# Optimization experiments

Measured on AMD Instinct MI355X. Metric: run time of the kernel, lower is better.

The kernel has to match this reference:

```python
import jax, jax.numpy as jnp
import numpy as np

B = 2; D = 256; NH = 8; NL = 4; HD = D // NH
K = 2; P = K * K; NV = 4; DFF = 1024
SHAPES = ((128, 128), (64, 64), (32, 32), (16, 16))
LV = sum(h * w for h, w in SHAPES)
START = np.cumsum([0] + [h * w for h, w in SHAPES])[:-1].tolist()
EPS = 1e-5

# fixed 2x2 sampling kernel, matching _create_kernel_indices (even kernel branch)
_ind = np.linspace(-0.5, 0.5, K)
_ii, _jj = np.meshgrid(_ind, _ind, indexing='ij')
KERNEL = jnp.asarray(np.stack([_jj, _ii], -1).reshape(-1, 2) / K, jnp.float32)  # (P,2)


def _layer_norm(x, w, b):
    m = x.mean(-1, keepdims=True)
    v = ((x - m) ** 2).mean(-1, keepdims=True)
    return (x - m) * jax.lax.rsqrt(v + EPS) * w + b


def _box_attention(query, value, ref_windows, vpw, vpb, opw, opb, boxw, boxb, attw, attb):
    b, lq, _ = query.shape
    # value projection, split into heads: (b, NH, LV, HD)
    v = (value @ vpw.T + vpb).reshape(b, LV, NH, HD).transpose(0, 2, 1, 3)

    # attention weights: softmax over all (level, point) jointly per head
    aw = query @ attw.T + attb
    aw = jax.nn.softmax(aw.reshape(b, lq, NH, NL * P), -1).reshape(b, lq, NH, NL, P)

    # where to attend (with_rotation=False -> 4 offset variables, angle from ref)
    ob = (query @ boxw.T + boxb).reshape(b, lq, NH, NL, NV)
    rw = ref_windows[:, :, None, None, :]                    # (b,lq,1,1,7)
    ref_boxes = rw[..., jnp.array([0, 1, 3, 4])]
    angles = jnp.broadcast_to(rw[..., 6:7], (b, lq, NH, NL, 1))
    boxes = ref_boxes + ob / 8.0 * ref_boxes[..., jnp.array([2, 3, 2, 3])]
    center = boxes[..., None, :2]                            # (b,lq,NH,NL,1,2)
    size = boxes[..., None, 2:]
    c, s = jnp.cos(angles), jnp.sin(angles)
    rot = jnp.stack([c, -s, s, c], -1).reshape(b, lq, NH, NL, 1, 2, 2)
    g = KERNEL * jax.nn.relu(size)                           # (b,lq,NH,NL,P,2)
    grid = center + (g[..., None, :] * rot).sum(-1)          # (b,lq,NH,NL,P,2)

    # multi-level bilinear sampling (= grid_sample align_corners=False, zero pad)
    bidx = jnp.arange(b)[:, None, None, None]
    hidx = jnp.arange(NH)[None, None, :, None]
    out = jnp.zeros((b, lq, NH, HD), v.dtype)
    for lvl, (H, W) in enumerate(SHAPES):
        st = START[lvl]
        vl = v[:, :, st:st + H * W]                          # (b,NH,HW,HD)
        loc = grid[:, :, :, lvl]                             # (b,lq,NH,P,2)
        x = loc[..., 0] * W - 0.5
        y = loc[..., 1] * H - 0.5
        x0f = jnp.floor(x); y0f = jnp.floor(y)
        wx = x - x0f; wy = y - y0f
        x0 = x0f.astype(jnp.int32); y0 = y0f.astype(jnp.int32)
        acc = jnp.zeros((b, lq, NH, P, HD), v.dtype)
        corners = ((0, 0, (1 - wx) * (1 - wy)), (1, 0, wx * (1 - wy)),
                   (0, 1, (1 - wx) * wy), (1, 1, wx * wy))
        for dx, dy, wgt in corners:
            xi = x0 + dx; yi = y0 + dy
            valid = (xi >= 0) & (xi < W) & (yi >= 0) & (yi < H)
            idx = jnp.clip(yi, 0, H - 1) * W + jnp.clip(xi, 0, W - 1)
            samp = vl[bidx, hidx, idx]                       # (b,lq,NH,P,HD)
            acc = acc + (wgt * valid)[..., None] * samp
        out = out + jnp.einsum('blhp,blhpd->blhd', aw[:, :, :, lvl], acc)
    return out.reshape(b, lq, D) @ opw.T + opb


def setup_inputs() -> dict:
    key = jax.random.key(0)
    ks = jax.random.split(key, 20)
    def nrm(k, shape, fan_in):
        return jax.random.normal(k, shape, jnp.float32) * (1.0 / np.sqrt(fan_in))
    rw = jax.random.uniform(ks[2], (B, LV, 7), jnp.float32)
    # keep window sizes (cols 3,4,5) modest, like real BEV reference windows
    rw = rw.at[..., 3:6].multiply(0.2)
    return {
        'src': jax.random.normal(ks[0], (B, LV, D), jnp.float32),
        'pos': jax.random.normal(ks[1], (B, LV, D), jnp.float32),
        'src_shape': jnp.asarray(SHAPES, jnp.int32),
        'src_start_idx': jnp.asarray(START, jnp.int32),
        'ref_windows': rw,
        'vpw': nrm(ks[3], (D, D), D), 'vpb': jnp.zeros((D,), jnp.float32),
        'opw': nrm(ks[4], (D, D), D), 'opb': jnp.zeros((D,), jnp.float32),
        'boxw': nrm(ks[5], (NL * NH * NV, D), D) * 0.1,
        'boxb': jax.random.normal(ks[6], (NL * NH * NV,), jnp.float32) * 0.1,
        'attw': nrm(ks[7], (NH * NL * P, D), D),
        'attb': jnp.zeros((NH * NL * P,), jnp.float32),
        'lin1_w': nrm(ks[8], (DFF, D), D), 'lin1_b': jnp.zeros((DFF,), jnp.float32),
        'lin2_w': nrm(ks[9], (D, DFF), DFF), 'lin2_b': jnp.zeros((D,), jnp.float32),
        'ln1_w': jnp.ones((D,), jnp.float32), 'ln1_b': jnp.zeros((D,), jnp.float32),
        'ln2_w': jnp.ones((D,), jnp.float32), 'ln2_b': jnp.zeros((D,), jnp.float32),
    }


def reference(src, pos, src_shape, src_start_idx, ref_windows,
              vpw, vpb, opw, opb, boxw, boxb, attw, attb,
              lin1_w, lin1_b, lin2_w, lin2_b, ln1_w, ln1_b, ln2_w, ln2_b):
    # level shapes/starts are static (SHAPES/START constants); src_shape /
    # src_start_idx are accepted for signature fidelity.
    src2 = _box_attention(src + pos, src, ref_windows,
                          vpw, vpb, opw, opb, boxw, boxb, attw, attb)
    src = _layer_norm(src + src2, ln1_w, ln1_b)
    ffn = jax.nn.relu(src @ lin1_w.T + lin1_b) @ lin2_w.T + lin2_b
    return _layer_norm(src + ffn, ln2_w, ln2_b)
```

## Files before the change

kernel.cpp:

```cpp
#include <hip/hip_runtime.h>
#include <stdint.h>

typedef unsigned short u16;
typedef __attribute__((ext_vector_type(8))) short short8;
typedef __attribute__((ext_vector_type(4))) float f32x4;

#define D_    256
#define NH_   8
#define HD_   32
#define LV_   21760
#define DFF_  1024
#define EPS_  1e-5f
#define MH_   21760
#define MT_   43520

__device__ __forceinline__ float bf2f(u16 u) {
    union { uint32_t i; float f; } x; x.i = ((uint32_t)u) << 16; return x.f;
}
__device__ __forceinline__ u16 f2bf(float f) {
    union { float f; uint32_t i; } x; x.f = f;
    uint32_t r = x.i + 0x7FFFu + ((x.i >> 16) & 1u);
    return (u16)(r >> 16);
}
__device__ __forceinline__ uint32_t pk2(float a, float b) {
    return (uint32_t)f2bf(a) | ((uint32_t)f2bf(b) << 16);
}
__device__ __forceinline__ float blo(uint32_t u) {
    union { uint32_t i; float f; } x; x.i = u << 16; return x.f;
}
__device__ __forceinline__ float bhi(uint32_t u) {
    union { uint32_t i; float f; } x; x.i = u & 0xffff0000u; return x.f;
}
__device__ __forceinline__ void cv8(u16* dst, float4 a, float4 b) {
    uint4 r;
    r.x = pk2(a.x, a.y); r.y = pk2(a.z, a.w);
    r.z = pk2(b.x, b.y); r.w = pk2(b.z, b.w);
    *(uint4*)dst = r;
}
__device__ __forceinline__ void gload16(const u16* g, u16* l) {
    __builtin_amdgcn_global_load_lds(
        (const __attribute__((address_space(1))) uint32_t*)g,
        (__attribute__((address_space(3))) uint32_t*)l, 16, 0, 0);
}

__global__ __launch_bounds__(256) void k_cvt2(const float* __restrict__ in1, u16* __restrict__ out1,
                                              const float* __restrict__ in2, u16* __restrict__ out2) {
    int i = blockIdx.x * 256 + threadIdx.x;
    const float* in = (i < 65536) ? in1 : in2;
    u16* out = (i < 65536) ? out1 : out2;
    const int j = i & 65535;
    float4 v = ((const float4*)in)[j];
    uint2 r; r.x = pk2(v.x, v.y); r.y = pk2(v.z, v.w);
    *(uint2*)(out + (size_t)j * 4) = r;
}

__global__ __launch_bounds__(256) void k_vproj(
        const float* __restrict__ src, const float* __restrict__ vpw,
        const float* __restrict__ vpb, u16* __restrict__ vout) {
    __shared__ u16 Asl[32 * 256];
    __shared__ u16 Bs[2][64 * 32];
    const int t = threadIdx.x;
    const int l = t & 63, w = t >> 6;
    const int m0 = blockIdx.x * 32;
    const int wm = w >> 1, wn = w & 1;
    const int fr = l & 15, fg = l >> 4;
    const int sr = t >> 2, sc = t & 3;
    const int wslot = sr * 32 + ((sc ^ ((sr >> 1) & 3)) << 3);
    const int b = m0 / LV_;

    #pragma unroll
    for (int i = 0; i < 4; ++i) {
        const int ii = t + i * 256;
        const int row = ii >> 5, c8 = ii & 31;
        const float* p = src + (size_t)(m0 + row) * 256 + c8 * 8;
        cv8(&Asl[row * 256 + ((c8 ^ (row & 15)) << 3)],
            *(const float4*)p, *(const float4*)(p + 4));
    }
    __syncthreads();

    for (int s = 0; s < 4; ++s) {
        const float* Bsl = vpw + (size_t)(s * 64) * 256;
        const float* gB = Bsl + (size_t)sr * 256 + sc * 8;
        f32x4 acc[2];
        acc[0] = (f32x4){0.f, 0.f, 0.f, 0.f};
        acc[1] = (f32x4){0.f, 0.f, 0.f, 0.f};
        cv8(&Bs[0][wslot], *(const float4*)gB, *(const float4*)(gB + 4));
        __syncthreads();
        for (int kt = 0; kt < 8; ++kt) {
            const int cur = kt & 1;
            float4 nb0, nb1;
            if (kt < 7) {
                nb0 = *(const float4*)(gB + (kt + 1) * 32);
                nb1 = *(const float4*)(gB + (kt + 1) * 32 + 4);
            }
            const int arow = wm * 16 + fr;
            const short8 af = *(const short8*)&Asl[arow * 256 + (((kt * 4 + fg) ^ (arow & 15)) << 3)];
            short8 bfr[2];
            #pragma unroll
            for (int ni = 0; ni < 2; ++ni) {
                const int r = wn * 32 + ni * 16 + fr;
                bfr[ni] = *(const short8*)&Bs[cur][r * 32 + ((fg ^ ((r >> 1) & 3)) << 3)];
            }
            #pragma unroll
            for (int ni = 0; ni < 2; ++ni)
                acc[ni] = __builtin_amdgcn_mfma_f32_16x16x32_bf16(af, bfr[ni], acc[ni], 0, 0, 0);
            if (kt < 7) {
                cv8(&Bs[cur ^ 1][wslot], nb0, nb1);
                __syncthreads();
            }
        }
        #pragma unroll
        for (int ni = 0; ni < 2; ++ni) {
            const int n = s * 64 + wn * 32 + ni * 16 + fr;
            const float bv = vpb[n];
            const int h = n >> 5, hd = n & 31;
            #pragma unroll
            for (int q = 0; q < 4; ++q) {
                const int m = m0 + wm * 16 + fg * 4 + q;
                const int lrow = m - b * LV_;
                vout[((size_t)(b * NH_ + h) * LV_ + lrow) * HD_ + hd] = f2bf(acc[ni][q] + bv);
            }
        }
    }
}

__global__ __launch_bounds__(256) void k_logits(
        const float* __restrict__ src, const float* __restrict__ pos,
        const float* __restrict__ attw, const float* __restrict__ attb,
        const float* __restrict__ boxw, const float* __restrict__ boxb,
        u16* __restrict__ lgout) {
    __shared__ u16 Asl[32 * 256];
    __shared__ u16 Bs[2][64 * 32];
    const int t = threadIdx.x;
    const int l = t & 63, w = t >> 6;
    const int m0 = blockIdx.x * 32;
    const int wm = w >> 1, wn = w & 1;
    const int fr = l & 15, fg = l >> 4;
    const int sr = t >> 2, sc = t & 3;
    const int wslot = sr * 32 + ((sc ^ ((sr >> 1) & 3)) << 3);

    #pragma unroll
    for (int i = 0; i < 4; ++i) {
        const int ii = t + i * 256;
        const int row = ii >> 5, c8 = ii & 31;
        const float* p  = src + (size_t)(m0 + row) * 256 + c8 * 8;
        const float* p2 = pos + (size_t)(m0 + row) * 256 + c8 * 8;
        float4 a0 = *(const float4*)p,  a1 = *(const float4*)(p + 4);
        float4 q0 = *(const float4*)p2, q1 = *(const float4*)(p2 + 4);
        a0.x += q0.x; a0.y += q0.y; a0.z += q0.z; a0.w += q0.w;
        a1.x += q1.x; a1.y += q1.y; a1.z += q1.z; a1.w += q1.w;
        cv8(&Asl[row * 256 + ((c8 ^ (row & 15)) << 3)], a0, a1);
    }
    __syncthreads();

    for (int s = 0; s < 4; ++s) {
        const float* Bsl = (s < 2) ? (attw + (size_t)(s * 64) * 256)
                                   : (boxw + (size_t)(s * 64 - 128) * 256);
        const float* gB = Bsl + (size_t)sr * 256 + sc * 8;
        f32x4 acc[2];
        acc[0] = (f32x4){0.f, 0.f, 0.f, 0.f};
        acc[1] = (f32x4){0.f, 0.f, 0.f, 0.f};
        cv8(&Bs[0][wslot], *(const float4*)gB, *(const float4*)(gB + 4));
        __syncthreads();
        for (int kt = 0; kt < 8; ++kt) {
            const int cur = kt & 1;
            float4 nb0, nb1;
            if (kt < 7) {
                nb0 = *(const float4*)(gB + (kt + 1) * 32);
                nb1 = *(const float4*)(gB + (kt + 1) * 32 + 4);
            }
            const int arow = wm * 16 + fr;
            const short8 af = *(const short8*)&Asl[arow * 256 + (((kt * 4 + fg) ^ (arow & 15)) << 3)];
            short8 bfr[2];
            #pragma unroll
            for (int ni = 0; ni < 2; ++ni) {
                const int r = wn * 32 + ni * 16 + fr;
                bfr[ni] = *(const short8*)&Bs[cur][r * 32 + ((fg ^ ((r >> 1) & 3)) << 3)];
            }
            #pragma unroll
            for (int ni = 0; ni < 2; ++ni)
                acc[ni] = __builtin_amdgcn_mfma_f32_16x16x32_bf16(af, bfr[ni], acc[ni], 0, 0, 0);
            if (kt < 7) {
                cv8(&Bs[cur ^ 1][wslot], nb0, nb1);
                __syncthreads();
            }
        }
        #pragma unroll
        for (int ni = 0; ni < 2; ++ni) {
            const int n = s * 64 + wn * 32 + ni * 16 + fr;
            const float bv = (n < 128) ? attb[n] : boxb[n - 128];
            const int off = (n < 128) ? ((n >> 4) * 32 + (n & 15))
                                      : (((n - 128) >> 4) * 32 + 16 + ((n - 128) & 15));
            #pragma unroll
            for (int q = 0; q < 4; ++q) {
                const int m = m0 + wm * 16 + fg * 4 + q;
                lgout[(size_t)m * 256 + off] = f2bf(acc[ni][q] + bv);
            }
        }
    }
}

__global__ __launch_bounds__(128, 8) void k_sample(
        const u16* __restrict__ lg, const float* __restrict__ refw,
        const u16* __restrict__ vws, u16* __restrict__ smp) {
    __shared__ float LG[8][2][36];
    __shared__ float RW[8][8];
    __shared__ __align__(16) uint2 CWI[16 * 68];
    const int t = threadIdx.x;
    const int bid = blockIdx.x;
    const int combo = bid & 7;
    const int idx = bid >> 3;
    const int b = combo >> 2, hp = combo & 3;
    const int h0 = hp * 2;
    const long gr0 = (long)b * LV_ + (long)idx * 8;
    const uint32_t PLANEB = (uint32_t)LV_ * HD_ * 2;

    {
        const int row = t >> 4, part = t & 15;
        const uint2 v = *(const uint2*)(lg + (size_t)(gr0 + row) * 256 + h0 * 32 + part * 4);
        const int hs = part >> 3, kk = (part & 7) * 4;
        LG[row][hs][kk]     = blo(v.x);
        LG[row][hs][kk + 1] = bhi(v.x);
        LG[row][hs][kk + 2] = blo(v.y);
        LG[row][hs][kk + 3] = bhi(v.y);
        if (t < 56) {
            int r2 = t / 7, k = t % 7;
            RW[r2][k] = refw[(gr0 + r2) * 7 + k];
        }
    }
    __syncthreads();
    if (t < 16) {
        const int row = t >> 1, hs = t & 1;
        float* a = LG[row][hs];
        float m = a[0];
        #pragma unroll
        for (int k = 1; k < 16; ++k) m = fmaxf(m, a[k]);
        float s = 0.f;
        float e[16];
        #pragma unroll
        for (int k = 0; k < 16; ++k) { e[k] = __expf(a[k] - m); s += e[k]; }
        const float inv = 1.f / s;
        #pragma unroll
        for (int k = 0; k < 16; ++k) a[k] = e[k] * inv;
    }
    __syncthreads();
    #pragma unroll
    for (int uu = 0; uu < 2; ++uu) {
        const int u = t + uu * 128;
        const int row = u >> 5, rem = u & 31;
        const int hs = rem >> 4, nl = (rem >> 2) & 3, p = rem & 3;
        const float rw0 = RW[row][0], rw1 = RW[row][1], rw3 = RW[row][3], rw4 = RW[row][4], ang = RW[row][6];
        const float ob0 = LG[row][hs][16 + nl * 4 + 0];
        const float ob1 = LG[row][hs][16 + nl * 4 + 1];
        const float ob2 = LG[row][hs][16 + nl * 4 + 2];
        const float ob3 = LG[row][hs][16 + nl * 4 + 3];
        const float cx = rw0 + ob0 * 0.125f * rw3;
        const float cy = rw1 + ob1 * 0.125f * rw4;
        const float bw = fmaxf(rw3 + ob2 * 0.125f * rw3, 0.f);
        const float bh = fmaxf(rw4 + ob3 * 0.125f * rw4, 0.f);
        const float kx = (p & 1) ? 0.25f : -0.25f;
        const float ky = (p >> 1) ? 0.25f : -0.25f;
        float sth, cth;
        __sincosf(ang, &sth, &cth);
        const float g0 = kx * bw, g1 = ky * bh;
        const float gx = cx + g0 * cth - g1 * sth;
        const float gy = cy + g0 * sth + g1 * cth;
        const int Wl = 128 >> nl;
        const int st = (65536 - (65536 >> (2 * nl))) / 3;
        const float x = gx * Wl - 0.5f, y = gy * Wl - 0.5f;
        const float xf = floorf(x), yf = floorf(y);
        const float wx = x - xf, wy = y - yf;
        const int x0 = (int)xf, y0 = (int)yf;
        const float awv = LG[row][hs][nl * 4 + p];
        const uint32_t hoff = hs ? PLANEB : 0u;
        uint2 cw[4];
        #pragma unroll
        for (int c4 = 0; c4 < 4; ++c4) {
            const int dx = c4 & 1, dy = c4 >> 1;
            const int xi = x0 + dx, yi = y0 + dy;
            const float wgt = (dx ? wx : 1.f - wx) * (dy ? wy : 1.f - wy);
            const bool valid = (xi >= 0) && (xi < Wl) && (yi >= 0) && (yi < Wl);
            const int xc = xi < 0 ? 0 : (xi > Wl - 1 ? Wl - 1 : xi);
            const int yc = yi < 0 ? 0 : (yi > Wl - 1 ? Wl - 1 : yi);
            const float wv = valid ? wgt * awv : 0.f;
            cw[c4].x = __float_as_uint(wv);
            cw[c4].y = (uint32_t)(st + yc * Wl + xc) * 64u + hoff;
        }
        const int g = row * 2 + hs, un = nl * 4 + p;
        uint2* d0 = &CWI[g * 68 + un * 2];
        *(uint4*)(d0)      = *(const uint4*)&cw[0];
        *(uint4*)(d0 + 34) = *(const uint4*)&cw[2];
    }
    __syncthreads();
    {
        const int e = t & 7, g = t >> 3;
        const int row = g >> 1, hs = g & 1;
        const char* vbp = (const char*)vws +
            (((size_t)(b * NH_ + h0) * LV_) * HD_ + e * 4) * 2;
        const uint2* cbase = &CWI[g * 68];
        float a0 = 0.f, a1 = 0.f, a2 = 0.f, a3 = 0.f;
        #pragma unroll 1
        for (int k = 0; k < 16; k += 2) {
            const uint4 c0 = *(const uint4*)&cbase[k * 2];
            const uint4 c1 = *(const uint4*)&cbase[34 + k * 2];
            const uint4 c2 = *(const uint4*)&cbase[(k + 1) * 2];
            const uint4 c3 = *(const uint4*)&cbase[34 + (k + 1) * 2];
            const uint2 d0 = *(const uint2*)(vbp + c0.y);
            const uint2 d1 = *(const uint2*)(vbp + c0.w);
            const uint2 d2 = *(const uint2*)(vbp + c1.y);
            const uint2 d3 = *(const uint2*)(vbp + c1.w);
            const uint2 d4 = *(const uint2*)(vbp + c2.y);
            const uint2 d5 = *(const uint2*)(vbp + c2.w);
            const uint2 d6 = *(const uint2*)(vbp + c3.y);
            const uint2 d7 = *(const uint2*)(vbp + c3.w);
            #define ACC8(WB, DD) do { \
                const float w_ = __uint_as_float(WB); \
                a0 += w_ * blo((DD).x); a1 += w_ * bhi((DD).x); \
                a2 += w_ * blo((DD).y); a3 += w_ * bhi((DD).y); \
            } while (0)
            ACC8(c0.x, d0); ACC8(c0.z, d1); ACC8(c1.x, d2); ACC8(c1.z, d3);
            ACC8(c2.x, d4); ACC8(c2.z, d5); ACC8(c3.x, d6); ACC8(c3.z, d7);
            #undef ACC8
        }
        uint2 o; o.x = pk2(a0, a1); o.y = pk2(a2, a3);
        *(uint2*)(smp + (size_t)(gr0 + row) * 256 + (h0 + hs) * 32 + e * 4) = o;
    }
}

__global__ __launch_bounds__(256) void k_oproj(
        const u16* __restrict__ A,
        const float* __restrict__ opw,
        const float* __restrict__ opb,
        const float* __restrict__ src,
        const float* __restrict__ lnw, const float* __restrict__ lnb,
        u16* __restrict__ out) {
    __shared__ char smem[36864];
    u16* As = (u16*)smem;
    u16* Bs = (u16*)(smem + 4096);
    float* Y = (float*)smem;
    const int t = threadIdx.x;
    const int l = t & 63, w = t >> 6;
    const int m0 = blockIdx.x * 32;
    const int sAr = t >> 2, sc = t & 3;
    const int aslot = sAr * 32 + ((sc ^ ((sAr >> 1) & 3)) << 3);
    const u16* gA = A + (size_t)(m0 + sAr) * 256 + sc * 8;
    const float* gB[4];
    int bslot[4];
    #pragma unroll
    for (int i = 0; i < 4; ++i) {
        const int r = (t >> 2) + i * 64;
        gB[i] = opw + (size_t)r * 256 + sc * 8;
        bslot[i] = r * 32 + ((sc ^ ((r >> 1) & 3)) << 3);
    }
    const int fr = l & 15, fg = l >> 4;

    f32x4 acc[2][4];
    #pragma unroll
    for (int mi = 0; mi < 2; ++mi)
        #pragma unroll
        for (int ni = 0; ni < 4; ++ni)
            acc[mi][ni] = (f32x4){0.f, 0.f, 0.f, 0.f};

    if (t < 128) *(uint4*)&As[aslot] = *(const uint4*)gA;
    #pragma unroll
    for (int i = 0; i < 4; ++i)
        cv8(&Bs[bslot[i]], *(const float4*)gB[i], *(const float4*)(gB[i] + 4));
    __syncthreads();

    for (int kt = 0; kt < 8; ++kt) {
        const int cur = kt & 1;
        uint4 na; float4 nb[4][2];
        if (kt < 7) {
            if (t < 128) na = *(const uint4*)(gA + (kt + 1) * 32);
            #pragma unroll
            for (int i = 0; i < 4; ++i) {
                nb[i][0] = *(const float4*)(gB[i] + (kt + 1) * 32);
                nb[i][1] = *(const float4*)(gB[i] + (kt + 1) * 32 + 4);
            }
        }
        short8 af[2], bfr[4];
        #pragma unroll
        for (int mi = 0; mi < 2; ++mi) {
            const int r = mi * 16 + fr;
            af[mi] = *(const short8*)&As[cur * 1024 + r * 32 + ((fg ^ ((r >> 1) & 3)) << 3)];
        }
        #pragma unroll
        for (int ni = 0; ni < 4; ++ni) {
            const int r = w * 64 + ni * 16 + fr;
            bfr[ni] = *(const short8*)&Bs[cur * 8192 + r * 32 + ((fg ^ ((r >> 1) & 3)) << 3)];
        }
        #pragma unroll
        for (int mi = 0; mi < 2; ++mi)
            #pragma unroll
            for (int ni = 0; ni < 4; ++ni)
                acc[mi][ni] = __builtin_amdgcn_mfma_f32_16x16x32_bf16(af[mi], bfr[ni], acc[mi][ni], 0, 0, 0);
        if (kt < 7) {
            if (t < 128) *(uint4*)&As[(cur ^ 1) * 1024 + aslot] = na;
            #pragma unroll
            for (int i = 0; i < 4; ++i)
                cv8(&Bs[(cur ^ 1) * 8192 + bslot[i]], nb[i][0], nb[i][1]);
            __syncthreads();
        }
    }
    __syncthreads();
    #pragma unroll
    for (int ni = 0; ni < 4; ++ni) {
        const int n = w * 64 + ni * 16 + fr;
        const float bv = opb[n];
        #pragma unroll
        for (int mi = 0; mi < 2; ++mi) {
            #pragma unroll
            for (int q = 0; q < 4; ++q) {
                const int ml = mi * 16 + fg * 4 + q;
                Y[ml * 256 + n] = acc[mi][ni][q] + bv + src[(size_t)(m0 + ml) * 256 + n];
            }
        }
    }
    __syncthreads();
    for (int rr = 0; rr < 8; ++rr) {
        const int m = w * 8 + rr;
        const float v0 = Y[m * 256 + l];
        const float v1 = Y[m * 256 + 64 + l];
        const float v2 = Y[m * 256 + 128 + l];
        const float v3 = Y[m * 256 + 192 + l];
        float s1 = v0 + v1 + v2 + v3;
        float s2 = v0 * v0 + v1 * v1 + v2 * v2 + v3 * v3;
        #pragma unroll
        for (int off = 32; off; off >>= 1) {
            s1 += __shfl_xor(s1, off);
            s2 += __shfl_xor(s2, off);
        }
        const float mean = s1 * (1.f / 256.f);
        const float var = s2 * (1.f / 256.f) - mean * mean;
        const float rs = rsqrtf(var + EPS_);
        const size_t ob = (size_t)(m0 + m) * 256;
        out[ob + l]       = f2bf((v0 - mean) * rs * lnw[l]       + lnb[l]);
        out[ob + 64 + l]  = f2bf((v1 - mean) * rs * lnw[64 + l]  + lnb[64 + l]);
        out[ob + 128 + l] = f2bf((v2 - mean) * rs * lnw[128 + l] + lnb[128 + l]);
        out[ob + 192 + l] = f2bf((v3 - mean) * rs * lnw[192 + l] + lnb[192 + l]);
    }
}

__global__ __launch_bounds__(256) void k_gemm1(
        const u16* __restrict__ A, const u16* __restrict__ Bw,
        const float* __restrict__ bias, u16* __restrict__ H) {
    __shared__ u16 As[2][128 * 32];
    __shared__ u16 Bs[2][128 * 32];
    const int t = threadIdx.x;
    const int l = t & 63, w = t >> 6;
    const int m0 = blockIdx.x * 128, n0 = blockIdx.y * 128;
    const int r0 = t >> 2, c0 = t & 3;
    const int gc = c0 ^ ((r0 >> 1) & 3);
    const u16* gA0 = A  + (size_t)(m0 + r0) * 256 + gc * 8;
    const u16* gA1 = A  + (size_t)(m0 + r0 + 64) * 256 + gc * 8;
    const u16* gB0 = Bw + (size_t)(n0 + r0) * 256 + gc * 8;
    const u16* gB1 = Bw + (size_t)(n0 + r0 + 64) * 256 + gc * 8;
    const int lbase = w * 512;
    const int fr = l & 15, fg = l >> 4;
    const int wm = w >> 1, wn = w & 1;

    f32x4 acc[4][4];
    #pragma unroll
    for (int mi = 0; mi < 4; ++mi)
        #pragma unroll
        for (int ni = 0; ni < 4; ++ni)
            acc[mi][ni] = (f32x4){0.f, 0.f, 0.f, 0.f};

    #define STAGE1(buf, kt) do { \
        gload16(gA0 + (kt) * 32, &As[buf][lbase]); \
        gload16(gA1 + (kt) * 32, &As[buf][2048 + lbase]); \
        gload16(gB0 + (kt) * 32, &Bs[buf][lbase]); \
        gload16(gB1 + (kt) * 32, &Bs[buf][2048 + lbase]); \
    } while (0)

    STAGE1(0, 0);
    __syncthreads();

    for (int kt = 0; kt < 8; ++kt) {
        const int cur = kt & 1;
        if (kt < 7) STAGE1(cur ^ 1, kt + 1);
        short8 af[4], bfr[4];
        #pragma unroll
        for (int mi = 0; mi < 4; ++mi) {
            const int r = wm * 64 + mi * 16 + fr;
            af[mi] = *(const short8*)&As[cur][r * 32 + ((fg ^ ((r >> 1) & 3)) << 3)];
        }
        #pragma unroll
        for (int ni = 0; ni < 4; ++ni) {
            const int r = wn * 64 + ni * 16 + fr;
            bfr[ni] = *(const short8*)&Bs[cur][r * 32 + ((fg ^ ((r >> 1) & 3)) << 3)];
        }
        #pragma unroll
        for (int mi = 0; mi < 4; ++mi)
            #pragma unroll
            for (int ni = 0; ni < 4; ++ni)
                acc[mi][ni] = __builtin_amdgcn_mfma_f32_16x16x32_bf16(af[mi], bfr[ni], acc[mi][ni], 0, 0, 0);
        __syncthreads();
    }
    #undef STAGE1
    #pragma unroll
    for (int ni = 0; ni < 4; ++ni) {
        const int n = n0 + wn * 64 + ni * 16 + fr;
        const float bv = bias[n];
        #pragma unroll
        for (int mi = 0; mi < 4; ++mi) {
            #pragma unroll
            for (int q = 0; q < 4; ++q) {
                const int m = m0 + wm * 64 + mi * 16 + fg * 4 + q;
                const float v = acc[mi][ni][q] + bv;
                H[(size_t)m * 1024 + n] = f2bf(fmaxf(v, 0.f));
            }
        }
    }
}

__global__ __launch_bounds__(256) void k_gemm2(
        const u16* __restrict__ A, const u16* __restrict__ Bw,
        const float* __restrict__ bias, const u16* __restrict__ resid,
        const float* __restrict__ lnw, const float* __restrict__ lnb,
        float* __restrict__ out) {
    __shared__ char smem[36864];
    u16* As = (u16*)smem;
    u16* Bs = (u16*)(smem + 4096);
    float* Y = (float*)smem;
    const int t = threadIdx.x;
    const int l = t & 63, w = t >> 6;
    const int m0 = blockIdx.x * 32;
    const int r0 = t >> 2, c0 = t & 3;
    const int gc = c0 ^ ((r0 >> 1) & 3);
    const u16* gA = A + (size_t)(m0 + r0) * 1024 + gc * 8;
    const u16* gBp[4];
    #pragma unroll
    for (int i = 0; i < 4; ++i)
        gBp[i] = Bw + (size_t)(i * 64 + r0) * 1024 + gc * 8;
    const int lbase = w * 512;
    const int fr = l & 15, fg = l >> 4;

    f32x4 acc[2][4];
    #pragma unroll
    for (int mi = 0; mi < 2; ++mi)
        #pragma unroll
        for (int ni = 0; ni < 4; ++ni)
            acc[mi][ni] = (f32x4){0.f, 0.f, 0.f, 0.f};

    #define STAGE2(buf, kt) do { \
        if (t < 128) gload16(gA + (kt) * 32, &As[(buf) * 1024 + lbase]); \
        gload16(gBp[0] + (kt) * 32, &Bs[(buf) * 8192 + lbase]); \
        gload16(gBp[1] + (kt) * 32, &Bs[(buf) * 8192 + 2048 + lbase]); \
        gload16(gBp[2] + (kt) * 32, &Bs[(buf) * 8192 + 4096 + lbase]); \
        gload16(gBp[3] + (kt) * 32, &Bs[(buf) * 8192 + 6144 + lbase]); \
    } while (0)

    STAGE2(0, 0);
    __syncthreads();

    for (int kt = 0; kt < 32; ++kt) {
        const int cur = kt & 1;
        if (kt < 31) STAGE2(cur ^ 1, kt + 1);
        short8 af[2], bfr[4];
        #pragma unroll
        for (int mi = 0; mi < 2; ++mi) {
            const int r = mi * 16 + fr;
            af[mi] = *(const short8*)&As[cur * 1024 + r * 32 + ((fg ^ ((r >> 1) & 3)) << 3)];
        }
        #pragma unroll
        for (int ni = 0; ni < 4; ++ni) {
            const int r = w * 64 + ni * 16 + fr;
            bfr[ni] = *(const short8*)&Bs[cur * 8192 + r * 32 + ((fg ^ ((r >> 1) & 3)) << 3)];
        }
        #pragma unroll
        for (int mi = 0; mi < 2; ++mi)
            #pragma unroll
            for (int ni = 0; ni < 4; ++ni)
                acc[mi][ni] = __builtin_amdgcn_mfma_f32_16x16x32_bf16(af[mi], bfr[ni], acc[mi][ni], 0, 0, 0);
        __syncthreads();
    }
    #undef STAGE2
    #pragma unroll
    for (int ni = 0; ni < 4; ++ni) {
        const int n = w * 64 + ni * 16 + fr;
        const float bv = bias[n];
        #pragma unroll
        for (int mi = 0; mi < 2; ++mi) {
            #pragma unroll
            for (int q = 0; q < 4; ++q) {
                const int ml = mi * 16 + fg * 4 + q;
                Y[ml * 256 + n] = acc[mi][ni][q] + bv + bf2f(resid[(size_t)(m0 + ml) * 256 + n]);
            }
        }
    }
    __syncthreads();
    for (int rr = 0; rr < 8; ++rr) {
        const int m = w * 8 + rr;
        const float v0 = Y[m * 256 + l];
        const float v1 = Y[m * 256 + 64 + l];
        const float v2 = Y[m * 256 + 128 + l];
        const float v3 = Y[m * 256 + 192 + l];
        float s1 = v0 + v1 + v2 + v3;
        float s2 = v0 * v0 + v1 * v1 + v2 * v2 + v3 * v3;
        #pragma unroll
        for (int off = 32; off; off >>= 1) {
            s1 += __shfl_xor(s1, off);
            s2 += __shfl_xor(s2, off);
        }
        const float mean = s1 * (1.f / 256.f);
        const float var = s2 * (1.f / 256.f) - mean * mean;
        const float rs = rsqrtf(var + EPS_);
        const size_t ob = (size_t)(m0 + m) * 256;
        out[ob + l]        = (v0 - mean) * rs * lnw[l]        + lnb[l];
        out[ob + 64 + l]   = (v1 - mean) * rs * lnw[64 + l]   + lnb[64 + l];
        out[ob + 128 + l]  = (v2 - mean) * rs * lnw[128 + l]  + lnb[128 + l];
        out[ob + 192 + l]  = (v3 - mean) * rs * lnw[192 + l]  + lnb[192 + l];
    }
}

extern "C" void kernel_launch(void* const* d_in, const int* in_sizes, int n_in,
                              void* d_out, int out_size, void* d_ws, size_t ws_size,
                              hipStream_t stream) {
    const float* src  = (const float*)d_in[0];
    const float* pos  = (const float*)d_in[1];
    const float* refw = (const float*)d_in[4];
    const float* vpw  = (const float*)d_in[5];
    const float* vpb  = (const float*)d_in[6];
    const float* opw  = (const float*)d_in[7];
    const float* opb  = (const float*)d_in[8];
    const float* boxw = (const float*)d_in[9];
    const float* boxb = (const float*)d_in[10];
    const float* attw = (const float*)d_in[11];
    const float* attb = (const float*)d_in[12];
    const float* l1w  = (const float*)d_in[13];
    const float* l1b  = (const float*)d_in[14];
    const float* l2w  = (const float*)d_in[15];
    const float* l2b  = (const float*)d_in[16];
    const float* ln1w = (const float*)d_in[17];
    const float* ln1b = (const float*)d_in[18];
    const float* ln2w = (const float*)d_in[19];
    const float* ln2b = (const float*)d_in[20];

    u16*   vws    = (u16*)d_ws;
    u16*   l1wb   = (u16*)d_ws;
    u16*   l2wb   = (u16*)((char*)d_ws + 524288);
    u16*   logitsb= (u16*)((char*)d_ws + 22282240u);
    u16*   src1b  = (u16*)((char*)d_ws + 22282240u);
    u16*   Hbf    = (u16*)((char*)d_ws + 44564480u);
    u16*   smp    = (u16*)((char*)d_ws + 66846720u);

    hipLaunchKernelGGL(k_vproj,  dim3(1360), dim3(256), 0, stream, src, vpw, vpb, vws);
    hipLaunchKernelGGL(k_logits, dim3(1360), dim3(256), 0, stream,
                       src, pos, attw, attb, boxw, boxb, logitsb);
    hipLaunchKernelGGL(k_sample, dim3(21760), dim3(128), 0, stream, logitsb, refw, vws, smp);
    hipLaunchKernelGGL(k_cvt2, dim3(512), dim3(256), 0, stream, l1w, l1wb, l2w, l2wb);
    hipLaunchKernelGGL(k_oproj, dim3(1360), dim3(256), 0, stream,
                       smp, opw, opb, src, ln1w, ln1b, src1b);
    for (int h = 0; h < 2; ++h) {
        const u16* Ah = src1b + (size_t)h * MH_ * 256;
        float* outh   = (float*)d_out + (size_t)h * MH_ * 256;
        hipLaunchKernelGGL(k_gemm1, dim3(170, 8), dim3(256), 0, stream, Ah, l1wb, l1b, Hbf);
        hipLaunchKernelGGL(k_gemm2, dim3(680), dim3(256), 0, stream, Hbf, l2wb, l2b, Ah, ln2w, ln2b, outh);
    }
}
```

Before: 321.8 us.

## Fuse FFN GEMMs into one kernel keeping hidden activations in shared memory

Replaces the two-kernel FFN (gemm1 writing a bf16 hidden buffer to global, then gemm2 reading it back) with a single kernel. Each 32-row block computes its hidden activations in 512-column halves, stores them in LDS and immediately runs the second GEMM on them, followed by the residual add and layernorm. This removes the global round trip for the large hidden tensor and several launches. The cost is that the first GEMM now uses small 32x64 tiles with a barrier per k-step and low MFMA count per sync, and 64KB of LDS per block may limit occupancy.

```diff
diff --git a/kernel.cpp b/kernel.cpp
--- a/kernel.cpp
+++ b/kernel.cpp
@@ -11,7 +11,6 @@
 #define LV_   21760
 #define DFF_  1024
 #define EPS_  1e-5f
-#define MH_   21760
 #define MT_   43520
 
 __device__ __forceinline__ float bf2f(u16 u) {
@@ -441,151 +440,131 @@
     }
 }
 
-__global__ __launch_bounds__(256) void k_gemm1(
-        const u16* __restrict__ A, const u16* __restrict__ Bw,
-        const float* __restrict__ bias, u16* __restrict__ H) {
-    __shared__ u16 As[2][128 * 32];
-    __shared__ u16 Bs[2][128 * 32];
-    const int t = threadIdx.x;
-    const int l = t & 63, w = t >> 6;
-    const int m0 = blockIdx.x * 128, n0 = blockIdx.y * 128;
-    const int r0 = t >> 2, c0 = t & 3;
-    const int gc = c0 ^ ((r0 >> 1) & 3);
-    const u16* gA0 = A  + (size_t)(m0 + r0) * 256 + gc * 8;
-    const u16* gA1 = A  + (size_t)(m0 + r0 + 64) * 256 + gc * 8;
-    const u16* gB0 = Bw + (size_t)(n0 + r0) * 256 + gc * 8;
-    const u16* gB1 = Bw + (size_t)(n0 + r0 + 64) * 256 + gc * 8;
-    const int lbase = w * 512;
-    const int fr = l & 15, fg = l >> 4;
-    const int wm = w >> 1, wn = w & 1;
-
-    f32x4 acc[4][4];
-    #pragma unroll
-    for (int mi = 0; mi < 4; ++mi)
-        #pragma unroll
-        for (int ni = 0; ni < 4; ++ni)
-            acc[mi][ni] = (f32x4){0.f, 0.f, 0.f, 0.f};
-
-    #define STAGE1(buf, kt) do { \
-        gload16(gA0 + (kt) * 32, &As[buf][lbase]); \
-        gload16(gA1 + (kt) * 32, &As[buf][2048 + lbase]); \
-        gload16(gB0 + (kt) * 32, &Bs[buf][lbase]); \
-        gload16(gB1 + (kt) * 32, &Bs[buf][2048 + lbase]); \
-    } while (0)
-
-    STAGE1(0, 0);
-    __syncthreads();
-
-    for (int kt = 0; kt < 8; ++kt) {
-        const int cur = kt & 1;
-        if (kt < 7) STAGE1(cur ^ 1, kt + 1);
-        short8 af[4], bfr[4];
-        #pragma unroll
-        for (int mi = 0; mi < 4; ++mi) {
-            const int r = wm * 64 + mi * 16 + fr;
-            af[mi] = *(const short8*)&As[cur][r * 32 + ((fg ^ ((r >> 1) & 3)) << 3)];
-        }
-        #pragma unroll
-        for (int ni = 0; ni < 4; ++ni) {
-            const int r = wn * 64 + ni * 16 + fr;
-            bfr[ni] = *(const short8*)&Bs[cur][r * 32 + ((fg ^ ((r >> 1) & 3)) << 3)];
-        }
-        #pragma unroll
-        for (int mi = 0; mi < 4; ++mi)
-            #pragma unroll
-            for (int ni = 0; ni < 4; ++ni)
-                acc[mi][ni] = __builtin_amdgcn_mfma_f32_16x16x32_bf16(af[mi], bfr[ni], acc[mi][ni], 0, 0, 0);
-        __syncthreads();
-    }
-    #undef STAGE1
-    #pragma unroll
-    for (int ni = 0; ni < 4; ++ni) {
-        const int n = n0 + wn * 64 + ni * 16 + fr;
-        const float bv = bias[n];
-        #pragma unroll
-        for (int mi = 0; mi < 4; ++mi) {
-            #pragma unroll
-            for (int q = 0; q < 4; ++q) {
-                const int m = m0 + wm * 64 + mi * 16 + fg * 4 + q;
-                const float v = acc[mi][ni][q] + bv;
-                H[(size_t)m * 1024 + n] = f2bf(fmaxf(v, 0.f));
-            }
-        }
-    }
-}
-
-__global__ __launch_bounds__(256) void k_gemm2(
-        const u16* __restrict__ A, const u16* __restrict__ Bw,
-        const float* __restrict__ bias, const u16* __restrict__ resid,
+__global__ __launch_bounds__(256) void k_ffn(
+        const u16* __restrict__ A,
+        const u16* __restrict__ l1wb,
+        const float* __restrict__ l1b,
+        const u16* __restrict__ l2wb,
+        const float* __restrict__ l2b,
         const float* __restrict__ lnw, const float* __restrict__ lnb,
         float* __restrict__ out) {
-    __shared__ char smem[36864];
-    u16* As = (u16*)smem;
-    u16* Bs = (u16*)(smem + 4096);
+    __shared__ u16 smem[32768];
+    u16* Hs  = smem;
+    u16* Asl = smem + 16384;
+    u16* B1  = smem + 24576;
+    u16* B2  = smem + 16384;
     float* Y = (float*)smem;
     const int t = threadIdx.x;
     const int l = t & 63, w = t >> 6;
     const int m0 = blockIdx.x * 32;
+    const int fr = l & 15, fg = l >> 4;
+    const int wm = w >> 1, wn = w & 1;
     const int r0 = t >> 2, c0 = t & 3;
-    const int gc = c0 ^ ((r0 >> 1) & 3);
-    const u16* gA = A + (size_t)(m0 + r0) * 1024 + gc * 8;
-    const u16* gBp[4];
-    #pragma unroll
-    for (int i = 0; i < 4; ++i)
-        gBp[i] = Bw + (size_t)(i * 64 + r0) * 1024 + gc * 8;
-    const int lbase = w * 512;
-    const int fr = l & 15, fg = l >> 4;
-
-    f32x4 acc[2][4];
+    const int gc2 = c0 ^ ((r0 >> 1) & 3);
+    const int aRowBase = 8 * w;
+    const int aSlot = l & 31;
+
+    f32x4 acc2[2][4];
     #pragma unroll
     for (int mi = 0; mi < 2; ++mi)
         #pragma unroll
         for (int ni = 0; ni < 4; ++ni)
-            acc[mi][ni] = (f32x4){0.f, 0.f, 0.f, 0.f};
-
-    #define STAGE2(buf, kt) do { \
-        if (t < 128) gload16(gA + (kt) * 32, &As[(buf) * 1024 + lbase]); \
-        gload16(gBp[0] + (kt) * 32, &Bs[(buf) * 8192 + lbase]); \
-        gload16(gBp[1] + (kt) * 32, &Bs[(buf) * 8192 + 2048 + lbase]); \
-        gload16(gBp[2] + (kt) * 32, &Bs[(buf) * 8192 + 4096 + lbase]); \
-        gload16(gBp[3] + (kt) * 32, &Bs[(buf) * 8192 + 6144 + lbase]); \
+            acc2[mi][ni] = (f32x4){0.f, 0.f, 0.f, 0.f};
+
+    #define STAGE_A() do { \
+        _Pragma("unroll") \
+        for (int j = 0; j < 4; ++j) { \
+            const int row = aRowBase + 2 * j + (l >> 5); \
+            const int c8 = aSlot ^ (row & 15); \
+            gload16(A + (size_t)(m0 + row) * 256 + c8 * 8, Asl + (aRowBase + 2 * j) * 256); \
+        } \
     } while (0)
-
-    STAGE2(0, 0);
-    __syncthreads();
-
-    for (int kt = 0; kt < 32; ++kt) {
-        const int cur = kt & 1;
-        if (kt < 31) STAGE2(cur ^ 1, kt + 1);
-        short8 af[2], bfr[4];
-        #pragma unroll
-        for (int mi = 0; mi < 2; ++mi) {
-            const int r = mi * 16 + fr;
-            af[mi] = *(const short8*)&As[cur * 1024 + r * 32 + ((fg ^ ((r >> 1) & 3)) << 3)];
-        }
-        #pragma unroll
-        for (int ni = 0; ni < 4; ++ni) {
-            const int r = w * 64 + ni * 16 + fr;
-            bfr[ni] = *(const short8*)&Bs[cur * 8192 + r * 32 + ((fg ^ ((r >> 1) & 3)) << 3)];
-        }
-        #pragma unroll
-        for (int mi = 0; mi < 2; ++mi)
-            #pragma unroll
-            for (int ni = 0; ni < 4; ++ni)
-                acc[mi][ni] = __builtin_amdgcn_mfma_f32_16x16x32_bf16(af[mi], bfr[ni], acc[mi][ni], 0, 0, 0);
+    #define STAGE_B1(buf, j0, kt) \
+        gload16(l1wb + (size_t)((j0) + r0) * 256 + (kt) * 32 + gc2 * 8, B1 + (buf) * 2048 + w * 512)
+    #define STAGE_B2(buf, kh, kt) do { \
+        _Pragma("unroll") \
+        for (int i = 0; i < 4; ++i) \
+            gload16(l2wb + (size_t)(i * 64 + r0) * 1024 + (kh) * 512 + (kt) * 32 + gc2 * 8, \
+                    B2 + (buf) * 8192 + i * 2048 + w * 512); \
+    } while (0)
+
+    STAGE_A();
+
+    for (int kh = 0; kh < 2; ++kh) {
+        if (kh == 1) STAGE_A();
+        for (int s = 0; s < 8; ++s) {
+            const int j0 = kh * 512 + s * 64;
+            f32x4 a1[2];
+            a1[0] = (f32x4){0.f, 0.f, 0.f, 0.f};
+            a1[1] = (f32x4){0.f, 0.f, 0.f, 0.f};
+            STAGE_B1(0, j0, 0);
+            __syncthreads();
+            for (int kt = 0; kt < 8; ++kt) {
+                const int cur = kt & 1;
+                if (kt < 7) STAGE_B1(cur ^ 1, j0, kt + 1);
+                const int arow = wm * 16 + fr;
+                const short8 af = *(const short8*)&Asl[arow * 256 + (((kt * 4 + fg) ^ (arow & 15)) << 3)];
+                short8 bfr[2];
+                #pragma unroll
+                for (int ni = 0; ni < 2; ++ni) {
+                    const int r = wn * 32 + ni * 16 + fr;
+                    bfr[ni] = *(const short8*)&B1[cur * 2048 + r * 32 + ((fg ^ ((r >> 1) & 3)) << 3)];
+                }
+                #pragma unroll
+                for (int ni = 0; ni < 2; ++ni)
+                    a1[ni] = __builtin_amdgcn_mfma_f32_16x16x32_bf16(af, bfr[ni], a1[ni], 0, 0, 0);
+                __syncthreads();
+            }
+            #pragma unroll
+            for (int ni = 0; ni < 2; ++ni) {
+                const int hc = s * 64 + wn * 32 + ni * 16 + fr;
+                const float bv = l1b[kh * 512 + hc];
+                #pragma unroll
+                for (int q = 0; q < 4; ++q) {
+                    const int hr = wm * 16 + fg * 4 + q;
+                    Hs[hr * 512 + (((hc >> 3) ^ (hr & 15)) << 3) + (hc & 7)] =
+                        f2bf(fmaxf(a1[ni][q] + bv, 0.f));
+                }
+            }
+        }
         __syncthreads();
-    }
-    #undef STAGE2
+        STAGE_B2(0, kh, 0);
+        __syncthreads();
+        for (int kt = 0; kt < 16; ++kt) {
+            const int cur = kt & 1;
+            if (kt < 15) STAGE_B2(cur ^ 1, kh, kt + 1);
+            short8 af2[2], bf2[4];
+            #pragma unroll
+            for (int mi = 0; mi < 2; ++mi) {
+                const int ar = mi * 16 + fr;
+                af2[mi] = *(const short8*)&Hs[ar * 512 + (((kt * 4 + fg) ^ (ar & 15)) << 3)];
+            }
+            #pragma unroll
+            for (int ni = 0; ni < 4; ++ni) {
+                const int r = w * 64 + ni * 16 + fr;
+                bf2[ni] = *(const short8*)&B2[cur * 8192 + r * 32 + ((fg ^ ((r >> 1) & 3)) << 3)];
+            }
+            #pragma unroll
+            for (int mi = 0; mi < 2; ++mi)
+                #pragma unroll
+                for (int ni = 0; ni < 4; ++ni)
+                    acc2[mi][ni] = __builtin_amdgcn_mfma_f32_16x16x32_bf16(af2[mi], bf2[ni], acc2[mi][ni], 0, 0, 0);
+            __syncthreads();
+        }
+    }
+    #undef STAGE_A
+    #undef STAGE_B1
+    #undef STAGE_B2
     #pragma unroll
     for (int ni = 0; ni < 4; ++ni) {
         const int n = w * 64 + ni * 16 + fr;
-        const float bv = bias[n];
+        const float bv = l2b[n];
         #pragma unroll
         for (int mi = 0; mi < 2; ++mi) {
             #pragma unroll
             for (int q = 0; q < 4; ++q) {
                 const int ml = mi * 16 + fg * 4 + q;
-                Y[ml * 256 + n] = acc[mi][ni][q] + bv + bf2f(resid[(size_t)(m0 + ml) * 256 + n]);
+                Y[ml * 256 + n] = acc2[mi][ni][q] + bv + bf2f(A[(size_t)(m0 + ml) * 256 + n]);
             }
         }
     }
@@ -642,7 +621,6 @@
     u16*   l2wb   = (u16*)((char*)d_ws + 524288);
     u16*   logitsb= (u16*)((char*)d_ws + 22282240u);
     u16*   src1b  = (u16*)((char*)d_ws + 22282240u);
-    u16*   Hbf    = (u16*)((char*)d_ws + 44564480u);
     u16*   smp    = (u16*)((char*)d_ws + 66846720u);
 
     hipLaunchKernelGGL(k_vproj,  dim3(1360), dim3(256), 0, stream, src, vpw, vpb, vws);
@@ -652,10 +630,6 @@
     hipLaunchKernelGGL(k_cvt2, dim3(512), dim3(256), 0, stream, l1w, l1wb, l2w, l2wb);
     hipLaunchKernelGGL(k_oproj, dim3(1360), dim3(256), 0, stream,
                        smp, opw, opb, src, ln1w, ln1b, src1b);
-    for (int h = 0; h < 2; ++h) {
-        const u16* Ah = src1b + (size_t)h * MH_ * 256;
-        float* outh   = (float*)d_out + (size_t)h * MH_ * 256;
-        hipLaunchKernelGGL(k_gemm1, dim3(170, 8), dim3(256), 0, stream, Ah, l1wb, l1b, Hbf);
-        hipLaunchKernelGGL(k_gemm2, dim3(680), dim3(256), 0, stream, Hbf, l2wb, l2b, Ah, ln2w, ln2b, outh);
-    }
-}
+    hipLaunchKernelGGL(k_ffn, dim3(1360), dim3(256), 0, stream,
+                       src1b, l1wb, l1b, l2wb, l2b, ln2w, ln2b, (float*)d_out);
+}
```

Measured after the change: 344.6 us. +7.1%, slower.
